# Kernel tuning notes

Hardware: AMD Instinct MI355X
Metric: run time of the kernel (lower is better)

The kernel has to match this reference:

```python
import jax, jax.numpy as jnp
import numpy as np

B, S, D_IN, D_OUT, R, E = 4, 2048, 2048, 2048, 16, 8
SCALING = 16.0 / 16.0  # lora_alpha / r


def setup_inputs() -> dict:
    key = jax.random.key(0)
    ks = jax.random.split(key, 5)
    x = jax.random.normal(ks[0], (B, S, D_IN), dtype=jnp.float32)
    W = jax.random.normal(ks[1], (D_OUT, D_IN), dtype=jnp.float32) * (1.0 / np.sqrt(D_IN))
    b = jax.random.normal(ks[2], (D_OUT,), dtype=jnp.float32) * 0.01
    lora_A = jax.random.normal(ks[3], (E, R, D_IN), dtype=jnp.float32) * (1.0 / np.sqrt(D_IN))
    lora_B = jax.random.normal(ks[4], (E, D_OUT, R), dtype=jnp.float32) * 0.01
    expert_mask = jnp.ones((E,), dtype=bool)
    return {"x": x, "W": W, "b": b, "lora_A": lora_A, "lora_B": lora_B, "expert_mask": expert_mask}


def reference(x, W, b, lora_A, lora_B, expert_mask):
    # Base linear: [B,S,D_in] @ [D_in,D_out]
    result = jnp.einsum('bsd,od->bso', x, W) + b
    # Masked sum over experts of B_e(A_e(x)) * scaling.
    # Collapse the per-expert sum: effective_A = sum over selected experts done via
    # masked contraction; since delta = sum_e m_e * (x A_e^T) B_e^T, fold mask into A.
    mA = lora_A * expert_mask.astype(x.dtype)[:, None, None]  # [E,R,D_in]
    z = jnp.einsum('bsd,erd->bser', x, mA)                     # [B,S,E,R]
    delta = jnp.einsum('bser,eor->bso', z, lora_B)             # [B,S,D_out]
    return result + delta * SCALING
```

## Files before the change

kernel.cpp:

```cpp
#include <hip/hip_runtime.h>
#include <stdint.h>

typedef __bf16 bf16x8 __attribute__((ext_vector_type(8)));
typedef float  f32x4  __attribute__((ext_vector_type(4)));
typedef float  float4v __attribute__((ext_vector_type(4)));
typedef short  short8 __attribute__((ext_vector_type(8)));
typedef short  short4v __attribute__((ext_vector_type(4)));

static constexpr int Mtot = 8192;
static constexpr int Ntot = 2048;
static constexpr int Ktot = 2048;
static constexpr int NE = 8, NR = 16;
static constexpr int R2 = NE * NR;
static constexpr float SCALING = 16.0f / 16.0f;

__device__ __forceinline__ ushort f2bf(float f) {
  union { float f; uint32_t u; } v; v.f = f;
  uint32_t r = (v.u + 0x7FFFu + ((v.u >> 16) & 1u)) >> 16;
  return (ushort)r;
}

__device__ __forceinline__ void lds16(const void* g, void* l) {
  __builtin_amdgcn_global_load_lds(
      (const __attribute__((address_space(1))) void*)g,
      (__attribute__((address_space(3))) void*)l, 16, 0, 0);
}

__global__ __launch_bounds__(256) void k_prep(const float* __restrict__ x,
                                              ushort* __restrict__ xb,
                                              const float* __restrict__ lA,
                                              const float* __restrict__ lB,
                                              const int* __restrict__ mask,
                                              ushort* __restrict__ Abt,
                                              ushort* __restrict__ Bst) {
  int tid = threadIdx.x;
  if (blockIdx.x < 8192) {
    size_t base = (size_t)blockIdx.x * 2048;
    int t4 = tid * 4;
    float4v a = *reinterpret_cast<const float4v*>(x + base + t4);
    float4v c = *reinterpret_cast<const float4v*>(x + base + 1024 + t4);
    short4v s0, s1;
    s0[0] = (short)f2bf(a[0]); s0[1] = (short)f2bf(a[1]);
    s0[2] = (short)f2bf(a[2]); s0[3] = (short)f2bf(a[3]);
    s1[0] = (short)f2bf(c[0]); s1[1] = (short)f2bf(c[1]);
    s1[2] = (short)f2bf(c[2]); s1[3] = (short)f2bf(c[3]);
    *reinterpret_cast<short4v*>(xb + base + t4) = s0;
    *reinterpret_cast<short4v*>(xb + base + 1024 + t4) = s1;
  } else if (blockIdx.x < 8200) {
    int d = (blockIdx.x - 8192) * 256 + tid;
    short8 buf[16];
    #pragma unroll 8
    for (int i = 0; i < R2; ++i)
      ((short*)buf)[i] = (short)f2bf(lA[(size_t)i * Ktot + d]);
    #pragma unroll
    for (int q = 0; q < 16; ++q)
      *reinterpret_cast<short8*>(Abt + (size_t)d * R2 + q * 8) = buf[q];
  } else {
    int o = (blockIdx.x - 8200) * 256 + tid;
    short8 buf[16];
    #pragma unroll
    for (int e = 0; e < NE; ++e) {
      float m = (mask[e] != 0) ? SCALING : 0.0f;
      #pragma unroll
      for (int rg = 0; rg < 4; ++rg) {
        float4v v = *reinterpret_cast<const float4v*>(lB + ((size_t)e * Ntot + o) * NR + rg * 4);
        ((short*)buf)[e * 16 + rg * 4 + 0] = (short)f2bf(v[0] * m);
        ((short*)buf)[e * 16 + rg * 4 + 1] = (short)f2bf(v[1] * m);
        ((short*)buf)[e * 16 + rg * 4 + 2] = (short)f2bf(v[2] * m);
        ((short*)buf)[e * 16 + rg * 4 + 3] = (short)f2bf(v[3] * m);
      }
    }
    #pragma unroll
    for (int q = 0; q < 16; ++q)
      *reinterpret_cast<short8*>(Bst + (size_t)o * R2 + q * 8) = buf[q];
  }
}

__global__ __launch_bounds__(256) void k_weff_mfma(const ushort* __restrict__ Bst,
                                                   const ushort* __restrict__ Abt,
                                                   const float* __restrict__ W,
                                                   ushort* __restrict__ Wb) {
  __shared__ __align__(128) char sA[32768];
  __shared__ __align__(128) char sB[32768];
  int bid = blockIdx.x;
  int o0 = (bid >> 4) * 128;
  int d0 = (bid & 15) * 128;
  int tid = threadIdx.x, w = tid >> 6, l = tid & 63;

  int srow = w * 32 + (l >> 4);
  int scolb = (l & 15) * 16;
  #pragma unroll
  for (int j = 0; j < 8; ++j) {
    int row = srow + j * 4;
    int colb = scolb ^ ((row & 7) << 4);
    lds16((const char*)Bst + (size_t)(o0 + row) * 256 + colb, sA + w * 8192 + j * 1024);
    lds16((const char*)Abt + (size_t)(d0 + row) * 256 + colb, sB + w * 8192 + j * 1024);
  }
  __syncthreads();

  int wr = w >> 1, wc = w & 1;
  int fr = l & 15;
  int fk16 = (l >> 4) * 16;
  int xm = (fr & 7) << 4;

  f32x4 acc[4][4];
  #pragma unroll
  for (int i = 0; i < 4; ++i)
    #pragma unroll
    for (int j = 0; j < 4; ++j) acc[i][j] = f32x4{0.f, 0.f, 0.f, 0.f};

  #pragma unroll
  for (int ks = 0; ks < 4; ++ks) {
    int kx = (ks * 64 + fk16) ^ xm;
    bf16x8 aF[4], bF[4];
    #pragma unroll
    for (int mi = 0; mi < 4; ++mi)
      aF[mi] = *reinterpret_cast<const bf16x8*>(sA + (wr * 64 + mi * 16 + fr) * 256 + kx);
    #pragma unroll
    for (int nj = 0; nj < 4; ++nj)
      bF[nj] = *reinterpret_cast<const bf16x8*>(sB + (wc * 64 + nj * 16 + fr) * 256 + kx);
    #pragma unroll
    for (int mi = 0; mi < 4; ++mi)
      #pragma unroll
      for (int nj = 0; nj < 4; ++nj)
        acc[mi][nj] = __builtin_amdgcn_mfma_f32_16x16x32_bf16(aF[mi], bF[nj], acc[mi][nj], 0, 0, 0);
  }

  int rr4 = (l >> 4) * 4;
  #pragma unroll
  for (int nj = 0; nj < 4; ++nj) {
    int col = d0 + wc * 64 + nj * 16 + fr;
    #pragma unroll
    for (int mi = 0; mi < 4; ++mi) {
      int row0 = o0 + wr * 64 + mi * 16 + rr4;
      #pragma unroll
      for (int r = 0; r < 4; ++r) {
        float v = acc[mi][nj][r] + W[(size_t)(row0 + r) * Ktot + col];
        Wb[(size_t)(row0 + r) * Ktot + col] = f2bf(v);
      }
    }
  }
}

__global__ __launch_bounds__(512, 2) void k_gemm256(const ushort* __restrict__ Xb,
                                                    const ushort* __restrict__ Wb,
                                                    const float* __restrict__ bias,
                                                    float* __restrict__ out) {
  constexpr int BK = 32;
  constexpr int NT = Ktot / BK;
  constexpr int NTN = Ntot / 256;
  __shared__ __align__(128) char smem[4 * 32768];

  int nwg = gridDim.x;
  int orig = blockIdx.x;
  int wg = (orig & 7) * (nwg >> 3) + (orig >> 3);
  int mBase = (wg / NTN) * 256;
  int nBase = (wg % NTN) * 256;

  int tid = threadIdx.x;
  int w = tid >> 6, l = tid & 63;
  int wr = w >> 2, wc = w & 3;

  int rowOff = tid >> 2;
  int cbS = ((tid & 3) * 16) ^ (((tid >> 3) & 3) << 4);
  const char* xbB = (const char*)Xb;
  const char* wbB = (const char*)Wb;
  const char* src[4];
  src[0] = xbB + (size_t)(mBase +       rowOff) * (Ktot * 2) + cbS;
  src[1] = xbB + (size_t)(mBase + 128 + rowOff) * (Ktot * 2) + cbS;
  src[2] = wbB + (size_t)(nBase +       rowOff) * (Ktot * 2) + cbS;
  src[3] = wbB + (size_t)(nBase + 128 + rowOff) * (Ktot * 2) + cbS;
  int waveB = w * 1024;

  auto stage = [&](int bufn, int which, size_t kb) {
    lds16(src[which] + kb, smem + bufn * 32768 + which * 8192 + waveB);
  };

  int fr = l & 15;
  int fkb = (l >> 4) * 16;
  int kx = fkb ^ (((fr >> 1) & 3) << 4);
  int aRd = (wr * 128 + fr) * 64 + kx;
  int bRd = 16384 + (wc * 64 + fr) * 64 + kx;

  f32x4 acc[8][4];
  #pragma unroll
  for (int i = 0; i < 8; ++i)
    #pragma unroll
    for (int j = 0; j < 4; ++j) acc[i][j] = f32x4{0.f, 0.f, 0.f, 0.f};

  bf16x8 aF[4], bF[4];

  #pragma unroll
  for (int q = 0; q < 4; ++q) stage(0, q, 0);
  #pragma unroll
  for (int q = 0; q < 4; ++q) stage(1, q, 64);
  __syncthreads();

  for (int t = 0; t < NT; ++t) {
    const char* buf = smem + (t & 3) * 32768;
    const bool pref = (t + 2 < NT);
    const int bn = (t + 2) & 3;
    const size_t kb = (size_t)(t + 2) * 64;

    #pragma unroll
    for (int mi = 0; mi < 4; ++mi)
      aF[mi] = *reinterpret_cast<const bf16x8*>(buf + aRd + mi * 1024);
    #pragma unroll
    for (int nj = 0; nj < 4; ++nj)
      bF[nj] = *reinterpret_cast<const bf16x8*>(buf + bRd + nj * 1024);
    if (pref) { stage(bn, 0, kb); stage(bn, 1, kb); }
    __builtin_amdgcn_s_barrier();
    __builtin_amdgcn_s_setprio(1);
    #pragma unroll
    for (int mi = 0; mi < 4; ++mi)
      #pragma unroll
      for (int nj = 0; nj < 4; ++nj)
        acc[mi][nj] = __builtin_amdgcn_mfma_f32_16x16x32_bf16(aF[mi], bF[nj], acc[mi][nj], 0, 0, 0);
    __builtin_amdgcn_s_setprio(0);
    __builtin_amdgcn_s_barrier();

    #pragma unroll
    for (int mi = 0; mi < 4; ++mi)
      aF[mi] = *reinterpret_cast<const bf16x8*>(buf + aRd + (4 + mi) * 1024);
    if (pref) { stage(bn, 2, kb); stage(bn, 3, kb); }
    __builtin_amdgcn_s_barrier();
    __builtin_amdgcn_s_setprio(1);
    #pragma unroll
    for (int mi = 0; mi < 4; ++mi)
      #pragma unroll
      for (int nj = 0; nj < 4; ++nj)
        acc[4 + mi][nj] = __builtin_amdgcn_mfma_f32_16x16x32_bf16(aF[mi], bF[nj], acc[4 + mi][nj], 0, 0, 0);
    __builtin_amdgcn_s_setprio(0);

    if (t + 2 < NT)      asm volatile("s_waitcnt vmcnt(4)" ::: "memory");
    else if (t + 1 < NT) asm volatile("s_waitcnt vmcnt(0)" ::: "memory");
    __builtin_amdgcn_s_barrier();
  }

  int rr = (l >> 4) * 4;
  #pragma unroll
  for (int nj = 0; nj < 4; ++nj) {
    int col = nBase + wc * 64 + nj * 16 + fr;
    float bb = bias[col];
    #pragma unroll
    for (int mi = 0; mi < 8; ++mi) {
      int row0 = mBase + wr * 128 + mi * 16 + rr;
      #pragma unroll
      for (int r = 0; r < 4; ++r)
        out[(size_t)(row0 + r) * Ntot + col] = acc[mi][nj][r] + bb;
    }
  }
}

extern "C" void kernel_launch(void* const* d_in, const int* in_sizes, int n_in,
                              void* d_out, int out_size, void* d_ws, size_t ws_size,
                              hipStream_t stream) {
  const float* x    = (const float*)d_in[0];
  const float* W    = (const float*)d_in[1];
  const float* bias = (const float*)d_in[2];
  const float* lA   = (const float*)d_in[3];
  const float* lB   = (const float*)d_in[4];
  const int*   mask = (const int*)d_in[5];
  float* out = (float*)d_out;

  ushort* xb  = (ushort*)d_ws;
  ushort* wb  = xb + (size_t)Mtot * Ktot;
  ushort* abt = wb + (size_t)Ntot * Ktot;
  ushort* bst = abt + (size_t)Ktot * R2;

  k_prep<<<8192 + 8 + 8, 256, 0, stream>>>(x, xb, lA, lB, mask, abt, bst);
  k_weff_mfma<<<(Ntot / 128) * (Ktot / 128), 256, 0, stream>>>(bst, abt, W, wb);
  k_gemm256<<<(Mtot / 256) * (Ntot / 256), 512, 0, stream>>>(xb, wb, bias, out);
}
```

Measured before the change: 213.3 us.

## Software-pipeline LDS fragment reads across K-tiles with ping-pong B registers

Restructures the GEMM main loop so the A-low and B fragments of the next K-tile are read from LDS while the current tile's second MFMA half runs, using ping-pong B register sets and a 2x unrolled loop. This cuts the per-tile barriers from three to one, with adjusted vmcnt waits. The aim is to hide LDS read latency and barrier stalls behind MFMA work, at the cost of more live registers and tighter hazard reasoning around the 4-buffer ring.

```diff
diff --git a/kernel.cpp b/kernel.cpp
--- a/kernel.cpp
+++ b/kernel.cpp
@@ -172,8 +172,8 @@
   src[3] = wbB + (size_t)(nBase + 128 + rowOff) * (Ktot * 2) + cbS;
   int waveB = w * 1024;
 
-  auto stage = [&](int bufn, int which, size_t kb) {
-    lds16(src[which] + kb, smem + bufn * 32768 + which * 8192 + waveB);
+  auto stage = [&](int bufn, int which, int tt) {
+    lds16(src[which] + (size_t)tt * 64, smem + bufn * 32768 + which * 8192 + waveB);
   };
 
   int fr = l & 15;
@@ -188,53 +188,64 @@
     #pragma unroll
     for (int j = 0; j < 4; ++j) acc[i][j] = f32x4{0.f, 0.f, 0.f, 0.f};
 
-  bf16x8 aF[4], bF[4];
+  bf16x8 aLo[4], aHi[4], bX[4], bY[4];
 
   #pragma unroll
   for (int q = 0; q < 4; ++q) stage(0, q, 0);
   #pragma unroll
-  for (int q = 0; q < 4; ++q) stage(1, q, 64);
+  for (int q = 0; q < 4; ++q) stage(1, q, 1);
+  asm volatile("s_waitcnt vmcnt(4)" ::: "memory");
   __syncthreads();
-
-  for (int t = 0; t < NT; ++t) {
-    const char* buf = smem + (t & 3) * 32768;
+  #pragma unroll
+  for (int nj = 0; nj < 4; ++nj)
+    bX[nj] = *reinterpret_cast<const bf16x8*>(smem + bRd + nj * 1024);
+  #pragma unroll
+  for (int mi = 0; mi < 4; ++mi)
+    aLo[mi] = *reinterpret_cast<const bf16x8*>(smem + aRd + mi * 1024);
+
+  auto tile_body = [&](int t, bf16x8 (&bCur)[4], bf16x8 (&bNxt)[4]) {
+    const char* buf  = smem + (t & 3) * 32768;
+    const char* bufN = smem + ((t + 1) & 3) * 32768;
     const bool pref = (t + 2 < NT);
     const int bn = (t + 2) & 3;
-    const size_t kb = (size_t)(t + 2) * 64;
-
-    #pragma unroll
-    for (int mi = 0; mi < 4; ++mi)
-      aF[mi] = *reinterpret_cast<const bf16x8*>(buf + aRd + mi * 1024);
-    #pragma unroll
-    for (int nj = 0; nj < 4; ++nj)
-      bF[nj] = *reinterpret_cast<const bf16x8*>(buf + bRd + nj * 1024);
-    if (pref) { stage(bn, 0, kb); stage(bn, 1, kb); }
+
+    if (pref) { stage(bn, 0, t + 2); stage(bn, 1, t + 2); }
+    #pragma unroll
+    for (int mi = 0; mi < 4; ++mi)
+      aHi[mi] = *reinterpret_cast<const bf16x8*>(buf + aRd + (4 + mi) * 1024);
+    __builtin_amdgcn_s_setprio(1);
+    #pragma unroll
+    for (int mi = 0; mi < 4; ++mi)
+      #pragma unroll
+      for (int nj = 0; nj < 4; ++nj)
+        acc[mi][nj] = __builtin_amdgcn_mfma_f32_16x16x32_bf16(aLo[mi], bCur[nj], acc[mi][nj], 0, 0, 0);
+    __builtin_amdgcn_s_setprio(0);
+
+    if (pref) asm volatile("s_waitcnt vmcnt(2)" ::: "memory");
+    else      asm volatile("s_waitcnt vmcnt(0)" ::: "memory");
     __builtin_amdgcn_s_barrier();
+    if (pref) { stage(bn, 2, t + 2); stage(bn, 3, t + 2); }
+
+    if (t + 1 < NT) {
+      #pragma unroll
+      for (int nj = 0; nj < 4; ++nj)
+        bNxt[nj] = *reinterpret_cast<const bf16x8*>(bufN + bRd + nj * 1024);
+      #pragma unroll
+      for (int mi = 0; mi < 4; ++mi)
+        aLo[mi] = *reinterpret_cast<const bf16x8*>(bufN + aRd + mi * 1024);
+    }
     __builtin_amdgcn_s_setprio(1);
     #pragma unroll
     for (int mi = 0; mi < 4; ++mi)
       #pragma unroll
       for (int nj = 0; nj < 4; ++nj)
-        acc[mi][nj] = __builtin_amdgcn_mfma_f32_16x16x32_bf16(aF[mi], bF[nj], acc[mi][nj], 0, 0, 0);
+        acc[4 + mi][nj] = __builtin_amdgcn_mfma_f32_16x16x32_bf16(aHi[mi], bCur[nj], acc[4 + mi][nj], 0, 0, 0);
     __builtin_amdgcn_s_setprio(0);
-    __builtin_amdgcn_s_barrier();
-
-    #pragma unroll
-    for (int mi = 0; mi < 4; ++mi)
-      aF[mi] = *reinterpret_cast<const bf16x8*>(buf + aRd + (4 + mi) * 1024);
-    if (pref) { stage(bn, 2, kb); stage(bn, 3, kb); }
-    __builtin_amdgcn_s_barrier();
-    __builtin_amdgcn_s_setprio(1);
-    #pragma unroll
-    for (int mi = 0; mi < 4; ++mi)
-      #pragma unroll
-      for (int nj = 0; nj < 4; ++nj)
-        acc[4 + mi][nj] = __builtin_amdgcn_mfma_f32_16x16x32_bf16(aF[mi], bF[nj], acc[4 + mi][nj], 0, 0, 0);
-    __builtin_amdgcn_s_setprio(0);
-
-    if (t + 2 < NT)      asm volatile("s_waitcnt vmcnt(4)" ::: "memory");
-    else if (t + 1 < NT) asm volatile("s_waitcnt vmcnt(0)" ::: "memory");
-    __builtin_amdgcn_s_barrier();
+  };
+
+  for (int t = 0; t < NT; t += 2) {
+    tile_body(t,     bX, bY);
+    tile_body(t + 1, bY, bX);
   }
 
   int rr = (l >> 4) * 4;
```

Result: no change. 213.7 us (+0.2%).
